# Optimization experiments

Measured on AMD Instinct MI355X. Metric: run time of the kernel, lower is better.

The kernel has to match this reference:

```python
import jax, jax.numpy as jnp
import numpy as np
from jax import lax


def conv2d(x, w, b, stride=1, pad=0):
    y = lax.conv_general_dilated(x, w, (stride, stride), [(pad, pad), (pad, pad)],
                                 dimension_numbers=('NCHW', 'OIHW', 'NCHW'))
    return y + b[None, :, None, None]


def squash(s, axis):
    # v = (|s|^2 / (1+|s|^2)) * s / |s|
    sq = jnp.sum(s * s, axis=axis, keepdims=True)
    return (sq / (1.0 + sq)) * s / jnp.sqrt(sq + 1e-9)


def conv_capsule(x, w, b_conv, caps_bias, out_dim, out_atoms, num_routing, stride, pad):
    # x: [B, in_dim, in_atoms, H, W]
    B, in_dim, in_atoms, H, W = x.shape
    xr = x.reshape(B * in_dim, in_atoms, H, W)
    conv = conv2d(xr, w, b_conv, stride, pad)              # [B*in_dim, out_dim*out_atoms, Ho, Wo]
    Ho, Wo = conv.shape[-2], conv.shape[-1]
    votes = conv.reshape(B, in_dim, out_dim, out_atoms, Ho, Wo)
    logits = jnp.zeros((B, in_dim, out_dim, Ho, Wo), dtype=x.dtype)
    act = None
    for i in range(num_routing):  # num_routing is a small static int (1 or 3)
        route = jax.nn.softmax(logits, axis=2)             # coupling over output capsules
        preact = jnp.einsum('bioHW,bioaHW->boaHW', route, votes) + caps_bias[None]
        act = squash(preact, axis=2)                        # [B, out_dim, out_atoms, Ho, Wo]
        if i < num_routing - 1:
            logits = logits + jnp.einsum('bioaHW,boaHW->bioHW', votes, act)
    return act


def forward(x, y, W1, b1, Wp, bp, cbp, Ws, bs, cbs, Wr1, br1, Wr2, br2, Wr3, br3):
    conv1 = jax.nn.relu(conv2d(x, W1, b1, 1, 2))                       # [B,256,H,W]
    primary = conv_capsule(conv1[:, None], Wp, bp, cbp, 32, 8, 1, 1, 2)  # [B,32,8,H,W]
    seg = conv_capsule(primary, Ws, bs, cbs, 1, 16, 3, 1, 0)             # [B,1,16,H,W]
    out_seg = jnp.sqrt(jnp.sum(seg * seg, axis=2) + 1e-9)                # Length: [B,1,H,W]
    masked = seg * y[:, :, None]                                         # Mask by label
    B, C, A, H, W = masked.shape
    r = masked.reshape(B * C, A, H, W)                                   # [B,16,H,W]
    r = jax.nn.relu(conv2d(r, Wr1, br1))
    r = jax.nn.relu(conv2d(r, Wr2, br2))
    out_recon = jax.nn.sigmoid(conv2d(r, Wr3, br3))                      # [B,1,H,W]
    return out_seg, out_recon


def setup_inputs():
    key = jax.random.key(0)
    ks = jax.random.split(key, 10)
    B, H, W = 2, 128, 128
    s = 0.05
    return {
        'x': jax.random.uniform(ks[0], (B, 1, H, W), jnp.float32),
        'y': (jax.random.uniform(ks[1], (B, 1, H, W)) > 0.5).astype(jnp.float32),
        'W1': jax.random.normal(ks[2], (256, 1, 5, 5), jnp.float32) * s,
        'b1': jnp.zeros((256,), jnp.float32),
        'Wp': jax.random.normal(ks[3], (256, 256, 5, 5), jnp.float32) * 0.01,
        'bp': jnp.zeros((256,), jnp.float32),
        'cbp': jnp.full((32, 8, 1, 1), 0.1, jnp.float32),
        'Ws': jax.random.normal(ks[4], (16, 8, 1, 1), jnp.float32) * s,
        'bs': jnp.zeros((16,), jnp.float32),
        'cbs': jnp.full((1, 16, 1, 1), 0.1, jnp.float32),
        'Wr1': jax.random.normal(ks[5], (64, 16, 1, 1), jnp.float32) * s,
        'br1': jnp.zeros((64,), jnp.float32),
        'Wr2': jax.random.normal(ks[6], (128, 64, 1, 1), jnp.float32) * s,
        'br2': jnp.zeros((128,), jnp.float32),
        'Wr3': jax.random.normal(ks[7], (1, 128, 1, 1), jnp.float32) * s,
        'br3': jnp.zeros((1,), jnp.float32),
    }


def reference(x, y, W1, b1, Wp, bp, cbp, Ws, bs, cbs, Wr1, br1, Wr2, br2, Wr3, br3):
    return forward(x, y, W1, b1, Wp, bp, cbp, Ws, bs, cbs, Wr1, br1, Wr2, br2, Wr3, br3)
```

## Files before the change

### kernel.cpp

```cpp
#include <hip/hip_runtime.h>
#include <hip/hip_bf16.h>

typedef __attribute__((ext_vector_type(8))) unsigned short us8;
typedef __attribute__((ext_vector_type(8))) __bf16 bf16x8;
typedef __attribute__((ext_vector_type(4))) float f32x4;

__device__ __forceinline__ unsigned short f2bf(float f) {
  unsigned int u = __float_as_uint(f);
  u += 0x7FFFu + ((u >> 16) & 1u);
  return (unsigned short)(u >> 16);
}
__device__ __forceinline__ float bf2f(unsigned short u) {
  return __uint_as_float(((unsigned int)u) << 16);
}

__device__ __forceinline__ void gld16(const unsigned short* g, unsigned short* l) {
  __builtin_amdgcn_global_load_lds(reinterpret_cast<const unsigned int*>(g),
                                   reinterpret_cast<unsigned int*>(l), 16, 0, 0);
}

#define APAD_BYTES 17842176
#define BT_OFF     17842176
#define PP_OFF     21118976

__global__ __launch_bounds__(256) void prep_halo(const float* __restrict__ Wp,
                                                 unsigned short* __restrict__ BT,
                                                 unsigned short* __restrict__ Apad) {
  __shared__ float w[6400];
  const int bid = blockIdx.x, tid = threadIdx.x;
  if (bid < 256) {
    const float* src = Wp + bid * 6400;
    for (int i = tid; i < 6400; i += 256) w[i] = src[i];
    __syncthreads();
    for (int k = tid; k < 6400; k += 256) {
      int dhw = k >> 8, c = k & 255;
      BT[bid * 6400 + k] = f2bf(w[c * 25 + dhw]);
    }
  } else {
    int idx = (bid - 256) * 256 + tid;
    int chunk = idx & 31;
    int pix = idx >> 5;
    int img = pix >= 1040;
    int p = pix - img * 1040;
    int h, w2;
    if (p < 528) {
      int rs = p / 132;
      h = (rs < 2) ? rs : rs + 128;
      w2 = p - rs * 132;
    } else {
      int q = p - 528;
      h = 2 + (q >> 2);
      int cs = q & 3;
      w2 = (cs < 2) ? cs : cs + 128;
    }
    us8 z = {0, 0, 0, 0, 0, 0, 0, 0};
    *(us8*)(Apad + (size_t)(img * 17424 + h * 132 + w2) * 256 + chunk * 8) = z;
  }
}

__global__ __launch_bounds__(256) void conv1_k(const float* __restrict__ x,
                                               const float* __restrict__ W1,
                                               const float* __restrict__ b1,
                                               unsigned short* __restrict__ Apad) {
  int t = threadIdx.x;
  int pxt = blockIdx.x >> 3;
  int cq  = blockIdx.x & 7;
  int px  = (pxt << 6) + (t & 63);
  int cg  = __builtin_amdgcn_readfirstlane(t >> 6);
  int co0 = (cq << 5) + (cg << 3);
  int b = px >> 14, hw = px & 16383;
  int h = hw >> 7, w = hw & 127;

  float patch[25];
#pragma unroll
  for (int dh = 0; dh < 5; ++dh)
#pragma unroll
    for (int dw = 0; dw < 5; ++dw) {
      int hh = h + dh - 2, ww = w + dw - 2;
      bool ok = (hh >= 0) & (hh < 128) & (ww >= 0) & (ww < 128);
      patch[dh * 5 + dw] = ok ? x[(b << 14) + hh * 128 + ww] : 0.f;
    }
  us8 o;
#pragma unroll
  for (int c = 0; c < 8; ++c) {
    float acc = b1[co0 + c];
#pragma unroll
    for (int i = 0; i < 25; ++i) acc += patch[i] * W1[(co0 + c) * 25 + i];
    o[c] = f2bf(fmaxf(acc, 0.f));
  }
  *(us8*)(Apad + (size_t)((b * 132 + h + 2) * 132 + (w + 2)) * 256 + co0) = o;
}

#define STAGE(slot, ku) do { int dhw_=(ku)>>3, dh_=dhw_/5, dw_=dhw_-dh_*5;     \
    int ao_=((dh_*132+dw_)<<8)+(((ku)&7)<<5);                                  \
    int kp_=(ku)<<5;                                                           \
    gld16(Aap+abase0+ao_, &As[slot][sA]);                                      \
    gld16(Aap+abase1+ao_, &As[slot][sA+4096]);                                 \
    gld16(BT+bbase0+kp_, &Bs[slot][sA]);                                       \
    gld16(BT+bbase1+kp_, &Bs[slot][sA+4096]); } while(0)
#define READ_SET(AST, BST, slot) do {                                          \
  _Pragma("unroll") for (int s_ = 0; s_ < 8; ++s_)                             \
    AST[s_] = *(const bf16x8*)(&As[slot][areadbase + s_*512]);                 \
  _Pragma("unroll") for (int j_ = 0; j_ < 4; ++j_)                             \
    BST[j_] = *(const bf16x8*)(&Bs[slot][breadbase + j_*512]); } while(0)
#define MFMA_SET(AST, BST) do {                                                \
  _Pragma("unroll") for (int s_ = 0; s_ < 8; ++s_)                             \
  _Pragma("unroll") for (int j_ = 0; j_ < 4; ++j_)                             \
    acc[s_][j_] = __builtin_amdgcn_mfma_f32_16x16x32_bf16(                     \
        AST[s_], BST[j_], acc[s_][j_], 0, 0, 0); } while(0)
#define BAR() __builtin_amdgcn_s_barrier()
#define VMC(n) asm volatile("s_waitcnt vmcnt(" #n ")" ::: "memory")
#define SB0() __builtin_amdgcn_sched_barrier(0)
#define SP(n) __builtin_amdgcn_s_setprio(n)

__global__ __launch_bounds__(512, 1) void caps_conv2(
    const unsigned short* __restrict__ Aap,
    const unsigned short* __restrict__ BT,
    unsigned short* __restrict__ Pp)
{
  __shared__ __attribute__((aligned(16))) unsigned short As[4][8192];
  __shared__ __attribute__((aligned(16))) unsigned short Bs[4][8192];

  const int tid = threadIdx.x;
  const int bid = blockIdx.x;
  const int lid = (bid & 7) * 32 + (bid >> 3);
  const int kid = lid & 1;
  const int m0 = (lid >> 1) << 8;
  const int t0 = kid * 100;
  const int wid = tid >> 6;
  const int l = tid & 63;

  const int swz = (l & 3) ^ ((l >> 3) & 3);
  int abase0, abase1, bbase0, bbase1;
  {
    int ra = wid * 16 + (l >> 2);
    int m = m0 + ra;
    int b = m >> 14, hw = m & 16383, h = hw >> 7, w = hw & 127;
    abase0 = ((b * 132 + h) * 132 + w) * 256 + swz * 8;
    m = m0 + ra + 128;
    b = m >> 14; hw = m & 16383; h = hw >> 7; w = hw & 127;
    abase1 = ((b * 132 + h) * 132 + w) * 256 + swz * 8;
    bbase0 = ra * 6400 + swz * 8;
    bbase1 = (ra + 128) * 6400 + swz * 8;
  }
  const int sA = wid * 512;

  const int rl = l & 15, q = l >> 4;
  const int wm = wid >> 2, wn = wid & 3;
  const int areadbase = (wm * 128 + rl) * 32 + ((q ^ ((rl >> 1) & 3)) << 3);
  const int breadbase = (wn * 64 + rl) * 32 + ((q ^ ((rl >> 1) & 3)) << 3);

  f32x4 acc[8][4] = {};
  bf16x8 aR0[8], bR0[4], aR1[8], bR1[4];

  STAGE(0, t0 + 0); STAGE(1, t0 + 1); STAGE(2, t0 + 2);
  VMC(4); BAR();
  READ_SET(aR0, bR0, 0);

  for (int it = 0; it < 48; ++it) {
    const int u = it * 2;
    READ_SET(aR1, bR1, (u + 1) & 3);
    STAGE((u + 3) & 3, t0 + u + 3);
    SP(1); MFMA_SET(aR0, bR0); SP(0);
    VMC(4); SB0(); BAR();
    READ_SET(aR0, bR0, (u + 2) & 3);
    STAGE((u + 4) & 3, t0 + u + 4);
    SP(1); MFMA_SET(aR1, bR1); SP(0);
    VMC(4); SB0(); BAR();
  }
  READ_SET(aR1, bR1, 1);
  STAGE(3, t0 + 99);
  SP(1); MFMA_SET(aR0, bR0); SP(0);
  VMC(4); SB0(); BAR();
  READ_SET(aR0, bR0, 2);
  SP(1); MFMA_SET(aR1, bR1); SP(0);
  VMC(0); SB0(); BAR();
  READ_SET(aR1, bR1, 3);
  SP(1); MFMA_SET(aR0, bR0); SP(0);
  MFMA_SET(aR1, bR1);

  unsigned short* P = Pp + kid * 8388608;
#pragma unroll
  for (int s = 0; s < 8; ++s) {
#pragma unroll
    for (int j = 0; j < 4; ++j) {
      int col = wn * 64 + j * 16 + rl;
      int mrow = m0 + wm * 128 + s * 16 + (q << 2);
#pragma unroll
      for (int e = 0; e < 4; ++e)
        P[(size_t)(mrow + e) * 256 + col] = f2bf(acc[s][j][e]);
    }
  }
}

__global__ __launch_bounds__(256) void tail_k3(
    const unsigned short* __restrict__ Pp, const float* __restrict__ y,
    const float* __restrict__ bp, const float* __restrict__ cbp,
    const float* __restrict__ Ws, const float* __restrict__ bs,
    const float* __restrict__ cbs,
    const float* __restrict__ Wr1, const float* __restrict__ br1,
    const float* __restrict__ Wr2, const float* __restrict__ br2,
    const float* __restrict__ Wr3, const float* __restrict__ br3,
    float* __restrict__ out) {
  __shared__ float ccl[256];
  __shared__ float sbl[16];
  __shared__ float Wsl[128];
  __shared__ float W1l[1024];
  __shared__ float b1l[64];
  __shared__ float W2l[8192];
  __shared__ float b2l[128];
  __shared__ float W3l[128];

  const int tid = threadIdx.x;
  ccl[tid] = bp[tid] * (1.f / 32.f) + cbp[tid];
  if (tid < 16) sbl[tid] = 32.f * bs[tid] + cbs[tid];
  if (tid < 128) { Wsl[tid] = Ws[tid]; b2l[tid] = br2[tid]; W3l[tid] = Wr3[tid]; }
  if (tid < 64) b1l[tid] = br1[tid];
  for (int i = tid; i < 1024; i += 256) W1l[i] = Wr1[i];
  for (int i = tid; i < 8192; i += 256) W2l[i] = Wr2[i];
  __syncthreads();

  const int m = blockIdx.x * 128 + (tid >> 1);
  const int hf = tid & 1;

  const us8* pr0 = (const us8*)(Pp + (size_t)m * 256) + hf * 16;
  const us8* pr1 = (const us8*)(Pp + 8388608 + (size_t)m * 256) + hf * 16;
  float P8[8] = {0.f, 0.f, 0.f, 0.f, 0.f, 0.f, 0.f, 0.f};
#pragma unroll 4
  for (int i = 0; i < 16; ++i) {
    us8 a = pr0[i], b = pr1[i];
    const int ci = (hf * 16 + i) * 8;
    float v[8];
#pragma unroll
    for (int c = 0; c < 8; ++c)
      v[c] = (bf2f(a[c]) + bf2f(b[c])) * (1.f / 32.f) + ccl[ci + c];
    float sqa = v[0]*v[0] + v[1]*v[1] + v[2]*v[2] + v[3]*v[3];
    float sqb = v[4]*v[4] + v[5]*v[5] + v[6]*v[6] + v[7]*v[7];
    float sq = sqa + sqb;
    float scale = sq / ((1.f + sq) * sqrtf(sq + 1e-9f));
#pragma unroll
    for (int c = 0; c < 8; ++c) P8[c] += v[c] * scale;
  }
#pragma unroll
  for (int c = 0; c < 8; ++c) P8[c] += __shfl_xor(P8[c], 1);

  float pre[16];
  float sqx = 0.f, sqy = 0.f;
#pragma unroll
  for (int a = 0; a < 16; ++a) {
    float s0 = P8[0]*Wsl[a*8+0] + P8[1]*Wsl[a*8+1] + P8[2]*Wsl[a*8+2] + P8[3]*Wsl[a*8+3];
    float s1 = P8[4]*Wsl[a*8+4] + P8[5]*Wsl[a*8+5] + P8[6]*Wsl[a*8+6] + P8[7]*Wsl[a*8+7];
    float s = sbl[a] + s0 + s1;
    pre[a] = s;
    if (a & 1) sqy += s * s; else sqx += s * s;
  }
  float sq2 = sqx + sqy;
  float sc2 = sq2 / ((1.f + sq2) * sqrtf(sq2 + 1e-9f));
  if (hf == 0) out[m] = sqrtf(sq2 * sc2 * sc2 + 1e-9f);

  const float f = sc2 * y[m];
  float r1o[32];
#pragma unroll
  for (int jj = 0; jj < 32; ++jj) {
    const float* wr = W1l + (hf * 32 + jj) * 16;
    float s0 = 0.f, s1 = 0.f;
#pragma unroll
    for (int a = 0; a < 8; ++a) { s0 += pre[a] * f * wr[a]; s1 += pre[a+8] * f * wr[a+8]; }
    r1o[jj] = fmaxf(b1l[hf * 32 + jj] + s0 + s1, 0.f);
  }
  float lo[32], hi[32];
#pragma unroll
  for (int jj = 0; jj < 32; ++jj) {
    float tmp = __shfl_xor(r1o[jj], 1);
    lo[jj] = hf ? tmp : r1o[jj];
    hi[jj] = hf ? r1o[jj] : tmp;
  }
  float a0 = 0.f, a1 = 0.f, a2 = 0.f, a3 = 0.f;
#pragma unroll 4
  for (int kk = 0; kk < 64; ++kk) {
    const int k = hf * 64 + kk;
    const float* w = W2l + k * 64;
    float s0 = 0.f, s1 = 0.f, s2 = 0.f, s3 = 0.f;
#pragma unroll
    for (int j = 0; j < 8; ++j) {
      s0 += lo[j] * w[j];        s1 += lo[j + 8] * w[j + 8];
      s2 += lo[j + 16] * w[j + 16]; s3 += lo[j + 24] * w[j + 24];
    }
#pragma unroll
    for (int j = 0; j < 8; ++j) {
      s0 += hi[j] * w[32 + j];        s1 += hi[j + 8] * w[40 + j];
      s2 += hi[j + 16] * w[48 + j];   s3 += hi[j + 24] * w[56 + j];
    }
    float s = b2l[k] + (s0 + s1) + (s2 + s3);
    float t = fmaxf(s, 0.f) * W3l[k];
    switch (kk & 3) { case 0: a0 += t; break; case 1: a1 += t; break;
                      case 2: a2 += t; break; default: a3 += t; }
  }
  float own = (a0 + a1) + (a2 + a3);
  float acc2 = br3[0] + own + __shfl_xor(own, 1);
  if (hf == 0) out[32768 + m] = 1.f / (1.f + expf(-acc2));
}

extern "C" void kernel_launch(void* const* d_in, const int* in_sizes, int n_in,
                              void* d_out, int out_size, void* d_ws, size_t ws_size,
                              hipStream_t stream) {
  const float* x   = (const float*)d_in[0];
  const float* y   = (const float*)d_in[1];
  const float* W1  = (const float*)d_in[2];
  const float* b1  = (const float*)d_in[3];
  const float* Wp  = (const float*)d_in[4];
  const float* bp  = (const float*)d_in[5];
  const float* cbp = (const float*)d_in[6];
  const float* Ws  = (const float*)d_in[7];
  const float* bs  = (const float*)d_in[8];
  const float* cbs = (const float*)d_in[9];
  const float* Wr1 = (const float*)d_in[10];
  const float* br1 = (const float*)d_in[11];
  const float* Wr2 = (const float*)d_in[12];
  const float* br2 = (const float*)d_in[13];
  const float* Wr3 = (const float*)d_in[14];
  const float* br3 = (const float*)d_in[15];
  float* out = (float*)d_out;

  char* ws = (char*)d_ws;
  unsigned short* Apad = (unsigned short*)ws;
  unsigned short* BT   = (unsigned short*)(ws + BT_OFF);
  unsigned short* Pp   = (unsigned short*)(ws + PP_OFF);

  hipLaunchKernelGGL(prep_halo, dim3(516), dim3(256), 0, stream, Wp, BT, Apad);
  hipLaunchKernelGGL(conv1_k, dim3(4096), dim3(256), 0, stream, x, W1, b1, Apad);
  hipLaunchKernelGGL(caps_conv2, dim3(256), dim3(512), 0, stream, Apad, BT, Pp);
  hipLaunchKernelGGL(tail_k3, dim3(256), dim3(256), 0, stream,
                     Pp, y, bp, cbp, Ws, bs, cbs, Wr1, br1, Wr2, br2, Wr3, br3, out);
}
```

Measured before the change: 154.8 us.

## Merge conv1 and prep kernels; load GEMM B operand directly into registers

Measured after the change: 203.8 us. 31.7% more time.

```diff
diff --git a/kernel.cpp b/kernel.cpp
--- a/kernel.cpp
+++ b/kernel.cpp
@@ -23,21 +23,52 @@
 #define BT_OFF     17842176
 #define PP_OFF     21118976
 
-__global__ __launch_bounds__(256) void prep_halo(const float* __restrict__ Wp,
-                                                 unsigned short* __restrict__ BT,
-                                                 unsigned short* __restrict__ Apad) {
+__global__ __launch_bounds__(256) void pre_k(const float* __restrict__ x,
+                                             const float* __restrict__ W1,
+                                             const float* __restrict__ b1,
+                                             const float* __restrict__ Wp,
+                                             unsigned short* __restrict__ BT,
+                                             unsigned short* __restrict__ Apad) {
   __shared__ float w[6400];
-  const int bid = blockIdx.x, tid = threadIdx.x;
-  if (bid < 256) {
-    const float* src = Wp + bid * 6400;
-    for (int i = tid; i < 6400; i += 256) w[i] = src[i];
+  const int bid = blockIdx.x, t = threadIdx.x;
+  if (bid < 4096) {
+    int pxt = bid >> 3;
+    int cq  = bid & 7;
+    int px  = (pxt << 6) + (t & 63);
+    int cg  = __builtin_amdgcn_readfirstlane(t >> 6);
+    int co0 = (cq << 5) + (cg << 3);
+    int b = px >> 14, hw = px & 16383;
+    int h = hw >> 7, wcol = hw & 127;
+
+    float patch[25];
+#pragma unroll
+    for (int dh = 0; dh < 5; ++dh)
+#pragma unroll
+      for (int dw = 0; dw < 5; ++dw) {
+        int hh = h + dh - 2, ww = wcol + dw - 2;
+        bool ok = (hh >= 0) & (hh < 128) & (ww >= 0) & (ww < 128);
+        patch[dh * 5 + dw] = ok ? x[(b << 14) + hh * 128 + ww] : 0.f;
+      }
+    us8 o;
+#pragma unroll
+    for (int c = 0; c < 8; ++c) {
+      float acc = b1[co0 + c];
+#pragma unroll
+      for (int i = 0; i < 25; ++i) acc += patch[i] * W1[(co0 + c) * 25 + i];
+      o[c] = f2bf(fmaxf(acc, 0.f));
+    }
+    *(us8*)(Apad + (size_t)((b * 132 + h + 2) * 132 + (wcol + 2)) * 256 + co0) = o;
+  } else if (bid < 4352) {
+    const int n = bid - 4096;
+    const float* src = Wp + n * 6400;
+    for (int i = t; i < 6400; i += 256) w[i] = src[i];
     __syncthreads();
-    for (int k = tid; k < 6400; k += 256) {
+    for (int k = t; k < 6400; k += 256) {
       int dhw = k >> 8, c = k & 255;
-      BT[bid * 6400 + k] = f2bf(w[c * 25 + dhw]);
+      BT[n * 6400 + k] = f2bf(w[c * 25 + dhw]);
     }
   } else {
-    int idx = (bid - 256) * 256 + tid;
+    int idx = (bid - 4352) * 256 + t;
     int chunk = idx & 31;
     int pix = idx >> 5;
     int img = pix >= 1040;
@@ -58,51 +89,18 @@
   }
 }
 
-__global__ __launch_bounds__(256) void conv1_k(const float* __restrict__ x,
-                                               const float* __restrict__ W1,
-                                               const float* __restrict__ b1,
-                                               unsigned short* __restrict__ Apad) {
-  int t = threadIdx.x;
-  int pxt = blockIdx.x >> 3;
-  int cq  = blockIdx.x & 7;
-  int px  = (pxt << 6) + (t & 63);
-  int cg  = __builtin_amdgcn_readfirstlane(t >> 6);
-  int co0 = (cq << 5) + (cg << 3);
-  int b = px >> 14, hw = px & 16383;
-  int h = hw >> 7, w = hw & 127;
-
-  float patch[25];
-#pragma unroll
-  for (int dh = 0; dh < 5; ++dh)
-#pragma unroll
-    for (int dw = 0; dw < 5; ++dw) {
-      int hh = h + dh - 2, ww = w + dw - 2;
-      bool ok = (hh >= 0) & (hh < 128) & (ww >= 0) & (ww < 128);
-      patch[dh * 5 + dw] = ok ? x[(b << 14) + hh * 128 + ww] : 0.f;
-    }
-  us8 o;
-#pragma unroll
-  for (int c = 0; c < 8; ++c) {
-    float acc = b1[co0 + c];
-#pragma unroll
-    for (int i = 0; i < 25; ++i) acc += patch[i] * W1[(co0 + c) * 25 + i];
-    o[c] = f2bf(fmaxf(acc, 0.f));
-  }
-  *(us8*)(Apad + (size_t)((b * 132 + h + 2) * 132 + (w + 2)) * 256 + co0) = o;
-}
-
-#define STAGE(slot, ku) do { int dhw_=(ku)>>3, dh_=dhw_/5, dw_=dhw_-dh_*5;     \
+#define STAGE_A(slot, ku) do { int dhw_=(ku)>>3, dh_=dhw_/5, dw_=dhw_-dh_*5;   \
     int ao_=((dh_*132+dw_)<<8)+(((ku)&7)<<5);                                  \
-    int kp_=(ku)<<5;                                                           \
     gld16(Aap+abase0+ao_, &As[slot][sA]);                                      \
-    gld16(Aap+abase1+ao_, &As[slot][sA+4096]);                                 \
-    gld16(BT+bbase0+kp_, &Bs[slot][sA]);                                       \
-    gld16(BT+bbase1+kp_, &Bs[slot][sA+4096]); } while(0)
-#define READ_SET(AST, BST, slot) do {                                          \
+    gld16(Aap+abase1+ao_, &As[slot][sA+4096]); } while(0)
+#define BLOADX(BST, u) do { const int kp_ = (t0+(u))<<5;                       \
+    BST[0] = *(const bf16x8*)(BTb + kp_);                                      \
+    BST[1] = *(const bf16x8*)(BTb + 102400 + kp_);                             \
+    BST[2] = *(const bf16x8*)(BTb + 204800 + kp_);                             \
+    BST[3] = *(const bf16x8*)(BTb + 307200 + kp_); } while(0)
+#define READ_A(AST, slot) do {                                                 \
   _Pragma("unroll") for (int s_ = 0; s_ < 8; ++s_)                             \
-    AST[s_] = *(const bf16x8*)(&As[slot][areadbase + s_*512]);                 \
-  _Pragma("unroll") for (int j_ = 0; j_ < 4; ++j_)                             \
-    BST[j_] = *(const bf16x8*)(&Bs[slot][breadbase + j_*512]); } while(0)
+    AST[s_] = *(const bf16x8*)(&As[slot][areadbase + s_*512]); } while(0)
 #define MFMA_SET(AST, BST) do {                                                \
   _Pragma("unroll") for (int s_ = 0; s_ < 8; ++s_)                             \
   _Pragma("unroll") for (int j_ = 0; j_ < 4; ++j_)                             \
@@ -119,7 +117,6 @@
     unsigned short* __restrict__ Pp)
 {
   __shared__ __attribute__((aligned(16))) unsigned short As[4][8192];
-  __shared__ __attribute__((aligned(16))) unsigned short Bs[4][8192];
 
   const int tid = threadIdx.x;
   const int bid = blockIdx.x;
@@ -131,7 +128,7 @@
   const int l = tid & 63;
 
   const int swz = (l & 3) ^ ((l >> 3) & 3);
-  int abase0, abase1, bbase0, bbase1;
+  int abase0, abase1;
   {
     int ra = wid * 16 + (l >> 2);
     int m = m0 + ra;
@@ -140,42 +137,46 @@
     m = m0 + ra + 128;
     b = m >> 14; hw = m & 16383; h = hw >> 7; w = hw & 127;
     abase1 = ((b * 132 + h) * 132 + w) * 256 + swz * 8;
-    bbase0 = ra * 6400 + swz * 8;
-    bbase1 = (ra + 128) * 6400 + swz * 8;
   }
   const int sA = wid * 512;
 
   const int rl = l & 15, q = l >> 4;
   const int wm = wid >> 2, wn = wid & 3;
   const int areadbase = (wm * 128 + rl) * 32 + ((q ^ ((rl >> 1) & 3)) << 3);
-  const int breadbase = (wn * 64 + rl) * 32 + ((q ^ ((rl >> 1) & 3)) << 3);
+  const unsigned short* BTb = BT + (wn * 64 + rl) * 6400 + q * 8;
 
   f32x4 acc[8][4] = {};
-  bf16x8 aR0[8], bR0[4], aR1[8], bR1[4];
-
-  STAGE(0, t0 + 0); STAGE(1, t0 + 1); STAGE(2, t0 + 2);
-  VMC(4); BAR();
-  READ_SET(aR0, bR0, 0);
+  bf16x8 aR0[8], aR1[8], bR0[4], bR1[4];
+
+  STAGE_A(0, t0 + 0); STAGE_A(1, t0 + 1); STAGE_A(2, t0 + 2);
+  BLOADX(bR0, 0);
+  VMC(8); BAR();
+  READ_A(aR0, 0);
 
   for (int it = 0; it < 48; ++it) {
     const int u = it * 2;
-    READ_SET(aR1, bR1, (u + 1) & 3);
-    STAGE((u + 3) & 3, t0 + u + 3);
+    BLOADX(bR1, u + 1);
+    READ_A(aR1, (u + 1) & 3);
+    STAGE_A((u + 3) & 3, t0 + u + 3);
     SP(1); MFMA_SET(aR0, bR0); SP(0);
-    VMC(4); SB0(); BAR();
-    READ_SET(aR0, bR0, (u + 2) & 3);
-    STAGE((u + 4) & 3, t0 + u + 4);
+    VMC(6); SB0(); BAR();
+    BLOADX(bR0, u + 2);
+    READ_A(aR0, (u + 2) & 3);
+    STAGE_A((u + 4) & 3, t0 + u + 4);
     SP(1); MFMA_SET(aR1, bR1); SP(0);
-    VMC(4); SB0(); BAR();
-  }
-  READ_SET(aR1, bR1, 1);
-  STAGE(3, t0 + 99);
+    VMC(6); SB0(); BAR();
+  }
+  BLOADX(bR1, 97);
+  READ_A(aR1, 1);
+  STAGE_A(3, t0 + 99);
   SP(1); MFMA_SET(aR0, bR0); SP(0);
+  VMC(6); SB0(); BAR();
+  BLOADX(bR0, 98);
+  READ_A(aR0, 2);
+  SP(1); MFMA_SET(aR1, bR1); SP(0);
   VMC(4); SB0(); BAR();
-  READ_SET(aR0, bR0, 2);
-  SP(1); MFMA_SET(aR1, bR1); SP(0);
-  VMC(0); SB0(); BAR();
-  READ_SET(aR1, bR1, 3);
+  BLOADX(bR1, 99);
+  READ_A(aR1, 3);
   SP(1); MFMA_SET(aR0, bR0); SP(0);
   MFMA_SET(aR1, bR1);
 
@@ -327,8 +328,7 @@
   unsigned short* BT   = (unsigned short*)(ws + BT_OFF);
   unsigned short* Pp   = (unsigned short*)(ws + PP_OFF);
 
-  hipLaunchKernelGGL(prep_halo, dim3(516), dim3(256), 0, stream, Wp, BT, Apad);
-  hipLaunchKernelGGL(conv1_k, dim3(4096), dim3(256), 0, stream, x, W1, b1, Apad);
+  hipLaunchKernelGGL(pre_k, dim3(4612), dim3(256), 0, stream, x, W1, b1, Wp, BT, Apad);
   hipLaunchKernelGGL(caps_conv2, dim3(256), dim3(512), 0, stream, Apad, BT, Pp);
   hipLaunchKernelGGL(tail_k3, dim3(256), dim3(256), 0, stream,
                      Pp, y, bp, cbp, Ws, bs, cbs, Wr1, br1, Wr2, br2, Wr3, br3, out);
```
